# Kernel tuning notes

Hardware: AMD Instinct MI355X
Metric: run time of the kernel (lower is better)

The kernel has to match this reference:

```python
import jax, jax.numpy as jnp
import numpy as np

N, E = 10000, 160000          # nodes, edges
MUL = 128                     # channel multiplicity of 0e and 1o blocks
NSP = 10                      # node_attrs (species one-hot) dim
NRAD = 8                      # edge_feats radial basis dim
SILU_C = 1.6790               # e3nn normalize2mom constant for SiLU
AVG_NEIGH = 16.0
SQ3 = np.sqrt(3.0).astype(np.float32)


def setup_inputs() -> dict:
    key = jax.random.key(0)
    ks = jax.random.split(key, 14)
    d = {}
    d["node_feats"] = jax.random.normal(ks[0], (N, 4 * MUL), jnp.float32)   # [N, 128 + 128*3]
    d["node_attrs"] = jax.random.normal(ks[1], (N, NSP), jnp.float32)
    d["edge_feats"] = jax.random.normal(ks[2], (E, NRAD), jnp.float32)
    d["edge_attrs"] = jax.random.normal(ks[3], (E, 4), jnp.float32)          # [0e | 1o]
    d["edge_index"] = jax.random.randint(ks[4], (2, E), 0, N, jnp.int32)
    # e3nn internal weights are standard normal; normalization applied in forward
    d["lin1_ws"] = jax.random.normal(ks[5], (MUL, MUL), jnp.float32)
    d["lin1_wv"] = jax.random.normal(ks[6], (MUL, MUL), jnp.float32)
    d["fc_w0"] = jax.random.normal(ks[7], (NRAD, 64), jnp.float32)
    d["fc_w1"] = jax.random.normal(ks[8], (64, 64), jnp.float32)
    d["fc_w2"] = jax.random.normal(ks[9], (64, 4 * MUL), jnp.float32)        # tp.weight_numel = 512
    d["lin2_ws"] = jax.random.normal(ks[10], (2 * MUL, MUL), jnp.float32)    # 256x0e -> 128x0e
    d["lin2_wv"] = jax.random.normal(ks[11], (2 * MUL, MUL), jnp.float32)    # 256x1o -> 128x1o
    d["sc_ws"] = jax.random.normal(ks[12], (MUL, NSP, MUL), jnp.float32)
    d["sc_wv"] = jax.random.normal(ks[13], (MUL, NSP, MUL), jnp.float32)
    return d


def _fc(ef, w0, w1, w2):
    # e3nn FullyConnectedNet: x @ W / sqrt(fan_in), normalize2mom-scaled SiLU between layers
    h = SILU_C * jax.nn.silu(ef @ w0 / np.float32(np.sqrt(NRAD)))
    h = SILU_C * jax.nn.silu(h @ w1 / np.float32(8.0))
    return h @ w2 / np.float32(8.0)


def reference(node_feats, node_attrs, edge_feats, edge_attrs, edge_index,
              lin1_ws, lin1_wv, fc_w0, fc_w1, fc_w2,
              lin2_ws, lin2_wv, sc_ws, sc_wv):
    x_s = node_feats[:, :MUL]                       # [N, 128] scalar block
    x_v = node_feats[:, MUL:].reshape(N, MUL, 3)    # [N, 128, 3] vector block

    # self-connection: FullyConnectedTensorProduct with 10x0e attrs; path weight 1/sqrt(mul1*mul2)
    sc_norm = np.float32(1.0 / np.sqrt(MUL * NSP))
    sc_s = jnp.einsum('nu,nv,uvw->nw', x_s, node_attrs, sc_ws) * sc_norm
    sc_v = jnp.einsum('nuc,nv,uvw->nwc', x_v, node_attrs, sc_wv) * sc_norm

    # linear_1 (per-irrep channel mixing, fan_in = 128)
    l1 = np.float32(1.0 / np.sqrt(MUL))
    y_s = (x_s @ lin1_ws) * l1
    y_v = jnp.einsum('nuc,uw->nwc', x_v, lin1_wv) * l1

    src = edge_index[1]
    dst = edge_index[0]
    xs_e = y_s[src]                                 # [E, 128]
    xv_e = y_v[src]                                 # [E, 128, 3]
    a_s = edge_attrs[:, :1]                         # [E, 1]
    a_v = edge_attrs[:, 1:]                         # [E, 3]

    w = _fc(edge_feats, fc_w0, fc_w1, fc_w2)        # [E, 512]
    w_ss, w_sv, w_vs, w_vv = jnp.split(w, 4, axis=1)  # instruction order in source

    # 'uvu' weighted tensor product with e3nn component/element normalization:
    # net coefficient per path works out to 1 except 1o x 1o -> 0e which is 1/sqrt(3)
    mid_s0 = w_ss * xs_e * a_s                                          # 0e*0e->0e
    mid_s1 = w_vv * jnp.einsum('euc,ec->eu', xv_e, a_v) / SQ3           # 1o*1o->0e
    mid_v2 = (w_sv * xs_e)[:, :, None] * a_v[:, None, :]                # 0e*1o->1o
    mid_v3 = w_vs[:, :, None] * xv_e * a_s[:, :, None]                  # 1o*0e->1o

    inv = np.float32(1.0 / np.sqrt(AVG_NEIGH))
    s = jax.ops.segment_sum(jnp.concatenate([mid_s0, mid_s1], axis=1), dst, num_segments=N) * inv  # [N, 256]
    v = jax.ops.segment_sum(jnp.concatenate([mid_v2, mid_v3], axis=1), dst, num_segments=N) * inv  # [N, 256, 3]

    # linear_2 (fan_in = 256)
    l2 = np.float32(1.0 / np.sqrt(2 * MUL))
    out_s = (s @ lin2_ws) * l2 + sc_s
    out_v = jnp.einsum('nuc,uw->nwc', v, lin2_wv) * l2 + sc_v

    return jnp.concatenate([out_s, out_v.reshape(N, 3 * MUL)], axis=1)   # [N, 512]
```

## Files before the change

### kernel.cpp

```cpp
#include <hip/hip_runtime.h>
#include <hip/hip_bf16.h>
#include <math.h>

#define N_NODES 10000
#define N_EDGES 160000
#define SO_BLK 157
#define VO_BLK 469

typedef __attribute__((ext_vector_type(8))) short short8x;
typedef __attribute__((ext_vector_type(4))) float floatx4;
typedef __attribute__((ext_vector_type(4))) unsigned int uint4x;
typedef __attribute__((ext_vector_type(2))) unsigned int uint2x;

union S8 { short8x v; unsigned short u[8]; uint4 q; uint4x qx; };
union U2 { uint2x v; unsigned short us[4]; };

__device__ __forceinline__ unsigned short f2bf(float x) {
    unsigned int u = __float_as_uint(x);
    return (unsigned short)((u + 0x7fffu + ((u >> 16) & 1u)) >> 16);
}
__device__ __forceinline__ float bf2f(unsigned short u) {
    return __uint_as_float(((unsigned)u) << 16);
}
__device__ __forceinline__ float silu_c(float x) {
    return 1.679f * x / (1.0f + __expf(-x));
}

__global__ __launch_bounds__(256) void pack_all_kernel(
    const float* __restrict__ sc_ws, const float* __restrict__ lin2_ws,
    const float* __restrict__ sc_wv, const float* __restrict__ lin2_wv,
    const float* __restrict__ fc_w2, const float* __restrict__ fc_w1,
    const float* __restrict__ lin1_ws, const float* __restrict__ lin1_wv,
    unsigned short* __restrict__ b_pre, unsigned short* __restrict__ w2a,
    unsigned short* __restrict__ w1a, unsigned short* __restrict__ b_lin)
{
    const int bid = blockIdx.x;
    const int t = threadIdx.x;
    if (bid < 192) {
        int id = bid * 256 + t;
        int mat = id / 24576;
        int slot = id - mat * 24576;
        int ks = slot >> 9;
        int rr = slot & 511;
        int lane = rr & 63;
        int quad = lane >> 4;
        int n = ((rr >> 6) << 4) + (lane & 15);
        const float* sc  = mat ? sc_wv  : sc_ws;
        const float* lin = mat ? lin2_wv : lin2_ws;
        S8 pk;
        #pragma unroll
        for (int j = 0; j < 8; j++) {
            int k = ks * 32 + quad * 8 + j;
            float w;
            if (k < 1280) {
                int u = k & 127, v = k >> 7;
                w = sc[(u * 10 + v) * 128 + n];
            } else {
                w = lin[(k - 1280) * 128 + n];
            }
            pk.u[j] = f2bf(w);
        }
        *(uint4*)(b_pre + (size_t)id * 8) = pk.q;
    } else if (bid < 208) {
        int id = (bid - 192) * 256 + t;
        int lane = id & 63;
        int mfg = (id >> 6) & 31;
        int ks = id >> 11;
        int col = mfg * 16 + (lane & 15);
        int k0 = ks * 32 + (lane >> 4) * 8;
        S8 pk;
        #pragma unroll
        for (int j = 0; j < 8; j++)
            pk.u[j] = f2bf(fc_w2[(k0 + j) * 512 + col] * 0.125f);
        *(uint4*)(w2a + (size_t)id * 8) = pk.q;
    } else if (bid < 210) {
        int id = (bid - 208) * 256 + t;
        int lane = id & 63;
        int mf = (id >> 6) & 3;
        int ks = id >> 8;
        int m = mf * 16 + (lane & 15);
        int k0 = ks * 32 + (lane >> 4) * 8;
        S8 pk;
        #pragma unroll
        for (int j = 0; j < 8; j++)
            pk.u[j] = f2bf(fc_w1[(k0 + j) * 64 + m] * 0.125f);
        *(uint4*)(w1a + (size_t)id * 8) = pk.q;
    } else {
        int id = (bid - 210) * 256 + t;
        int mat = id >> 11;
        int slot = id & 2047;
        int ks = slot >> 9;
        int rr = slot & 511;
        int nf = rr >> 6;
        int lane = rr & 63;
        int n = nf * 16 + (lane & 15);
        int k0 = ks * 32 + (lane >> 4) * 8;
        const float* w = mat ? lin1_wv : lin1_ws;
        const float l1 = 0.0883883476483f;
        S8 pk;
        #pragma unroll
        for (int j = 0; j < 8; j++)
            pk.u[j] = f2bf(w[(k0 + j) * 128 + n] * l1);
        *(uint4*)(b_lin + (size_t)id * 8) = pk.q;
    }
}

__global__ __launch_bounds__(256) void node_lin1_mfma(
    const float* __restrict__ node_feats,
    const unsigned short* __restrict__ b_lin,
    unsigned short* __restrict__ y_pk,
    unsigned short* __restrict__ xvP16)
{
    __shared__ __align__(16) unsigned char smem[32768];
    short8x* Al = (short8x*)smem;
    unsigned short* Yt = (unsigned short*)smem;

    const int blk = blockIdx.x;
    const int t = threadIdx.x;
    const int base = blk * 32;
    const int lane = t & 63;
    const int wv = t >> 6;
    const int m15 = lane & 15;
    const int k0q = (lane >> 4) * 8;

    #pragma unroll
    for (int it = 0; it < 8; it++) {
        int g = wv * 8 + it;
        int af = g >> 2;
        int ks = g & 3;
        int m = af * 16 + m15;
        int comp = m >> 5;
        int nloc = m & 31;
        int node = base + nloc;
        int valid = (node < N_NODES);
        if (!valid) node = N_NODES - 1;
        int k0 = ks * 32 + k0q;
        const float* row = node_feats + (size_t)node * 512;
        S8 pk;
        if (comp == 0) {
            float4 a = *(const float4*)&row[k0];
            float4 b = *(const float4*)&row[k0 + 4];
            pk.u[0] = f2bf(a.x); pk.u[1] = f2bf(a.y); pk.u[2] = f2bf(a.z); pk.u[3] = f2bf(a.w);
            pk.u[4] = f2bf(b.x); pk.u[5] = f2bf(b.y); pk.u[6] = f2bf(b.z); pk.u[7] = f2bf(b.w);
        } else {
            int c = comp - 1;
            #pragma unroll
            for (int j = 0; j < 8; j++)
                pk.u[j] = f2bf(row[128 + (k0 + j) * 3 + c]);
            if (valid)
                *(uint4*)&xvP16[((size_t)node * 3 + c) * 128 + k0] = pk.q;
        }
        Al[(ks * 8 + af) * 64 + lane] = pk.v;
    }
    __syncthreads();

    floatx4 c[8][2];
    #pragma unroll
    for (int af = 0; af < 8; af++) {
        c[af][0] = (floatx4){0.f, 0.f, 0.f, 0.f};
        c[af][1] = (floatx4){0.f, 0.f, 0.f, 0.f};
    }

    const uint4* bq = (const uint4*)b_lin;
    #pragma unroll
    for (int ks = 0; ks < 4; ks++) {
        S8 bs0, bs1, bv0, bv1;
        bs0.q = bq[       ks*512 + (wv*2+0)*64 + lane];
        bs1.q = bq[       ks*512 + (wv*2+1)*64 + lane];
        bv0.q = bq[2048 + ks*512 + (wv*2+0)*64 + lane];
        bv1.q = bq[2048 + ks*512 + (wv*2+1)*64 + lane];
        #pragma unroll
        for (int af = 0; af < 8; af++) {
            short8x a = Al[(ks*8 + af)*64 + lane];
            if (af < 2) {
                c[af][0] = __builtin_amdgcn_mfma_f32_16x16x32_bf16(a, bs0.v, c[af][0], 0, 0, 0);
                c[af][1] = __builtin_amdgcn_mfma_f32_16x16x32_bf16(a, bs1.v, c[af][1], 0, 0, 0);
            } else {
                c[af][0] = __builtin_amdgcn_mfma_f32_16x16x32_bf16(a, bv0.v, c[af][0], 0, 0, 0);
                c[af][1] = __builtin_amdgcn_mfma_f32_16x16x32_bf16(a, bv1.v, c[af][1], 0, 0, 0);
            }
        }
    }
    __syncthreads();

    {
        const int rq = (lane >> 4) * 4;
        #pragma unroll
        for (int af = 0; af < 8; af++) {
            #pragma unroll
            for (int nf = 0; nf < 2; nf++) {
                int u = wv * 32 + nf * 16 + m15;
                #pragma unroll
                for (int i = 0; i < 4; i++) {
                    int m = af * 16 + rq + i;
                    int comp = m >> 5, nloc = m & 31;
                    Yt[(nloc * 128 + u) * 4 + comp] = f2bf(c[af][nf][i]);
                }
            }
        }
    }
    __syncthreads();
    {
        unsigned short* dst = y_pk + (size_t)base * 512;
        int nrem = N_NODES - base;
        #pragma unroll
        for (int it = 0; it < 8; it++) {
            int idx = it * 256 + t;
            if ((idx >> 6) < nrem)
                *(uint4*)(dst + (size_t)idx * 8) = *(const uint4*)&Yt[idx * 8];
        }
    }
}

__global__ __launch_bounds__(256) void hist_kernel(const int* __restrict__ edge_index,
                                                   int* __restrict__ deg) {
    int e = blockIdx.x * 256 + threadIdx.x;
    if (e < N_EDGES) atomicAdd(&deg[edge_index[e]], 1);
}

__global__ __launch_bounds__(1024) void scan_kernel(const int* __restrict__ deg,
                                                    int* __restrict__ row_start,
                                                    int* __restrict__ cursor) {
    __shared__ int wsum[16];
    __shared__ int carry_s;
    const int t = threadIdx.x;
    const int lane = t & 63, w = t >> 6;
    if (t == 0) carry_s = 0;
    __syncthreads();
    for (int chunk = 0; chunk < 10; chunk++) {
        int idx = chunk * 1024 + t;
        int v = (idx < N_NODES) ? deg[idx] : 0;
        int x = v;
        #pragma unroll
        for (int off = 1; off < 64; off <<= 1) {
            int yv = __shfl_up(x, off, 64);
            if (lane >= off) x += yv;
        }
        if (lane == 63) wsum[w] = x;
        __syncthreads();
        int wpre = 0;
        for (int i = 0; i < w; i++) wpre += wsum[i];
        int incl = x + wpre + carry_s;
        int excl = incl - v;
        if (idx < N_NODES) { row_start[idx] = excl; cursor[idx] = excl; }
        __syncthreads();
        if (t == 1023) carry_s = incl;
        __syncthreads();
    }
    if (t == 0) row_start[N_NODES] = carry_s;
}

__global__ __launch_bounds__(256) void scatter_kernel(const int* __restrict__ edge_index,
                                                      const float* __restrict__ edge_attrs,
                                                      int* __restrict__ cursor,
                                                      int* __restrict__ edge_list,
                                                      int* __restrict__ srcs,
                                                      float* __restrict__ ea_sorted) {
    int e = blockIdx.x * 256 + threadIdx.x;
    if (e < N_EDGES) {
        int pos = atomicAdd(&cursor[edge_index[e]], 1);
        edge_list[pos] = e;
        srcs[pos] = edge_index[N_EDGES + e];
        float4 ea = *(const float4*)(edge_attrs + (size_t)e * 4);
        *(float4*)(ea_sorted + (size_t)pos * 4) = ea;
    }
}

__global__ __launch_bounds__(256) void edge_w_mfma(
    const float* __restrict__ edge_feats,
    const int* __restrict__ edge_list,
    const float* __restrict__ fc_w0,
    const unsigned short* __restrict__ w1a,
    const unsigned short* __restrict__ w2a,
    unsigned short* __restrict__ w_pk)
{
    __shared__ __align__(16) unsigned char smem[26368];
    float* ef = (float*)smem;
    unsigned short* h0b = (unsigned short*)(smem + 2304);
    unsigned short* T   = (unsigned short*)smem;
    unsigned short* h1b = (unsigned short*)(smem + 16896);
    int* eids = (int*)(smem + 26112);

    const int blk = blockIdx.x;
    const int t = threadIdx.x;
    const int eb0 = blk * 64;
    const int lane = t & 63;
    const int wv = t >> 6;
    const int quad = lane >> 4;
    const int m15 = lane & 15;

    if (t < 64) eids[t] = edge_list[eb0 + t];
    __syncthreads();

    #pragma unroll
    for (int r = 0; r < 2; r++) {
        int idx = r * 256 + t;
        int el = idx >> 3;
        int k = idx & 7;
        ef[el * 9 + k] = edge_feats[(size_t)eids[el] * 8 + k];
    }
    __syncthreads();

    {
        const int e_loc = t >> 2;
        const int c0 = (t & 3) * 16;
        float a0[16];
        #pragma unroll
        for (int i = 0; i < 16; i++) a0[i] = 0.f;
        const float* efr = &ef[e_loc * 9];
        #pragma unroll
        for (int k = 0; k < 8; k++) {
            float ek = efr[k];
            float w[16];
            #pragma unroll
            for (int q4 = 0; q4 < 4; q4++)
                *(float4*)&w[q4*4] = *(const float4*)&fc_w0[k*64 + c0 + q4*4];
            #pragma unroll
            for (int i = 0; i < 16; i++) a0[i] += ek * w[i];
        }
        const float is8 = 0.35355339059f;
        S8 p0, p1;
        #pragma unroll
        for (int i = 0; i < 8; i++) {
            p0.u[i] = f2bf(silu_c(a0[i] * is8));
            p1.u[i] = f2bf(silu_c(a0[8 + i] * is8));
        }
        *(uint4*)&h0b[e_loc * 72 + c0]     = p0.q;
        *(uint4*)&h0b[e_loc * 72 + c0 + 8] = p1.q;
    }
    __syncthreads();

    {
        floatx4 c2[4];
        #pragma unroll
        for (int ee = 0; ee < 4; ee++) c2[ee] = (floatx4){0.f, 0.f, 0.f, 0.f};
        const uint4* w1aq = (const uint4*)w1a;
        #pragma unroll
        for (int ks = 0; ks < 2; ks++) {
            S8 afr;
            afr.q = w1aq[(ks*4 + wv)*64 + lane];
            #pragma unroll
            for (int ee = 0; ee < 4; ee++) {
                S8 bfr;
                bfr.q = *(const uint4*)&h0b[(ee*16 + m15) * 72 + ks*32 + quad*8];
                c2[ee] = __builtin_amdgcn_mfma_f32_16x16x32_bf16(afr.v, bfr.v, c2[ee], 0, 0, 0);
            }
        }
        #pragma unroll
        for (int ee = 0; ee < 4; ee++) {
            ushort4 pk = make_ushort4(f2bf(silu_c(c2[ee][0])), f2bf(silu_c(c2[ee][1])),
                                      f2bf(silu_c(c2[ee][2])), f2bf(silu_c(c2[ee][3])));
            *(ushort4*)&h1b[(ee*16 + m15) * 72 + wv*16 + quad*4] = pk;
        }
    }
    __syncthreads();

    const uint4* w2aq = (const uint4*)w2a;
    #pragma unroll 1
    for (int p = 0; p < 4; p++) {
        floatx4 c3[2][4];
        #pragma unroll
        for (int mf = 0; mf < 2; mf++)
            #pragma unroll
            for (int ee = 0; ee < 4; ee++)
                c3[mf][ee] = (floatx4){0.f, 0.f, 0.f, 0.f};

        #pragma unroll
        for (int ks = 0; ks < 2; ks++) {
            S8 bfr[4];
            #pragma unroll
            for (int ee = 0; ee < 4; ee++)
                bfr[ee].q = *(const uint4*)&h1b[(ee*16 + m15) * 72 + ks*32 + quad*8];
            #pragma unroll
            for (int mf = 0; mf < 2; mf++) {
                S8 afr;
                afr.q = w2aq[(size_t)(ks*32 + wv*8 + p*2 + mf) * 64 + lane];
                #pragma unroll
                for (int ee = 0; ee < 4; ee++)
                    c3[mf][ee] = __builtin_amdgcn_mfma_f32_16x16x32_bf16(afr.v, bfr[ee].v, c3[mf][ee], 0, 0, 0);
            }
        }

        __syncthreads();
        #pragma unroll
        for (int mf = 0; mf < 2; mf++) {
            #pragma unroll
            for (int ee = 0; ee < 4; ee++) {
                int e = ee*16 + m15;
                #pragma unroll
                for (int i = 0; i < 4; i++) {
                    int colp = mf*16 + quad*4 + i;
                    T[e*132 + colp*4 + wv] = f2bf(c3[mf][ee][i]);
                }
            }
        }
        __syncthreads();

        #pragma unroll
        for (int it = 0; it < 8; it++) {
            int idx = it * 256 + t;
            int e  = idx >> 5;
            int cu = idx & 31;
            uint2x v = *(const uint2x*)&T[e*132 + cu*4];
            unsigned short* dstp = w_pk + ((size_t)(eb0 + e) * 128 + p*32 + cu) * 4;
            *(uint2x*)dstp = v;
        }
    }
}

__global__ __launch_bounds__(256) void gather_kernel(
    const int* __restrict__ row_start,
    const int* __restrict__ srcs,
    const float* __restrict__ ea_sorted,
    const unsigned short* __restrict__ w_pk,
    const unsigned short* __restrict__ y_pk,
    float* __restrict__ accS,
    float* __restrict__ accV)
{
    const int t = threadIdx.x;
    const int wv = t >> 6;
    const int n = blockIdx.x * 2 + (wv >> 1);
    const int lane = t & 63;
    const int u = ((wv & 1) << 6) + lane;

    const int eb = row_start[n];
    const int ee = row_start[n + 1];

    float aS0=0.f, aS1=0.f;
    float aV2x=0.f, aV2y=0.f, aV2z=0.f;
    float aV3x=0.f, aV3y=0.f, aV3z=0.f;

    auto consume = [&](const U2& w8, const U2& y8, const float4& ea) {
        float wss = bf2f(w8.us[0]), wsv = bf2f(w8.us[1]);
        float wvs = bf2f(w8.us[2]), wvv = bf2f(w8.us[3]);
        float qs = bf2f(y8.us[0]), q0 = bf2f(y8.us[1]), q1 = bf2f(y8.us[2]), q2 = bf2f(y8.us[3]);
        aS0 += wss * qs * ea.x;
        aS1 += wvv * (q0*ea.y + q1*ea.z + q2*ea.w);
        float tsv = wsv * qs;
        aV2x += tsv * ea.y; aV2y += tsv * ea.z; aV2z += tsv * ea.w;
        float tvs = wvs * ea.x;
        aV3x += tvs * q0; aV3y += tvs * q1; aV3z += tvs * q2;
    };

    if (eb < ee) {
        const int lastE = ee - 1;
        int j1 = (eb+1 < lastE) ? eb+1 : lastE;
        int sA = srcs[eb];
        int sB = srcs[j1];
        int sP0 = srcs[(eb+2 < lastE) ? eb+2 : lastE];
        int sP1 = srcs[(eb+3 < lastE) ? eb+3 : lastE];

        U2 wA, wB, yA, yB; float4 eaA, eaB;
        wA.v = __builtin_nontemporal_load((const uint2x*)(w_pk + ((size_t)eb * 128 + u) * 4));
        eaA  = *(const float4*)(ea_sorted + (size_t)eb * 4);
        yA.v = *(const uint2x*)(y_pk + ((size_t)sA * 128 + u) * 4);
        wB.v = __builtin_nontemporal_load((const uint2x*)(w_pk + ((size_t)j1 * 128 + u) * 4));
        eaB  = *(const float4*)(ea_sorted + (size_t)j1 * 4);
        yB.v = *(const uint2x*)(y_pk + ((size_t)sB * 128 + u) * 4);

        for (int i = eb; i < ee; i += 2) {
            consume(wA, yA, eaA);
            {
                int jn = (i+2 < lastE) ? i+2 : lastE;
                wA.v = __builtin_nontemporal_load((const uint2x*)(w_pk + ((size_t)jn * 128 + u) * 4));
                eaA  = *(const float4*)(ea_sorted + (size_t)jn * 4);
                yA.v = *(const uint2x*)(y_pk + ((size_t)sP0 * 128 + u) * 4);
                sP0 = srcs[(i+4 < lastE) ? i+4 : lastE];
            }
            if (i + 1 < ee) consume(wB, yB, eaB);
            {
                int jn = (i+3 < lastE) ? i+3 : lastE;
                wB.v = __builtin_nontemporal_load((const uint2x*)(w_pk + ((size_t)jn * 128 + u) * 4));
                eaB  = *(const float4*)(ea_sorted + (size_t)jn * 4);
                yB.v = *(const uint2x*)(y_pk + ((size_t)sP1 * 128 + u) * 4);
                sP1 = srcs[(i+5 < lastE) ? i+5 : lastE];
            }
        }
    }

    const float inv = 0.25f;
    const float s1c = 0.57735026919f * 0.25f;
    accS[(size_t)n*256 + u]       = aS0 * inv;
    accS[(size_t)n*256 + 128 + u] = aS1 * s1c;
    accV[((size_t)n*3+0)*256 + u]       = aV2x * inv;
    accV[((size_t)n*3+0)*256 + 128 + u] = aV3x * inv;
    accV[((size_t)n*3+1)*256 + u]       = aV2y * inv;
    accV[((size_t)n*3+1)*256 + 128 + u] = aV3y * inv;
    accV[((size_t)n*3+2)*256 + u]       = aV2z * inv;
    accV[((size_t)n*3+2)*256 + 128 + u] = aV3z * inv;
}

__global__ __launch_bounds__(256) void node_out_mfma(
    const float* __restrict__ node_feats,
    const float* __restrict__ node_attrs,
    const unsigned short* __restrict__ xvP16,
    const float* __restrict__ accS,
    const float* __restrict__ accV,
    const unsigned short* __restrict__ b_pre,
    float* __restrict__ out)
{
    __shared__ __align__(16) short8x Abuf[2][256];
    const int bid = blockIdx.x;
    const int t = threadIdx.x;
    const int lane = t & 63;
    const int wv = t >> 6;
    const bool is_s = (bid < SO_BLK);

    const int r    = ((t >> 6) << 4) + (t & 15);
    const int q8   = ((t >> 4) & 3) * 8;

    const float* px = nullptr;
    const unsigned short* pxv = nullptr;
    const float* pa;
    const float* pat;
    if (is_s) {
        int R = bid * 64 + r;
        int node = (R < N_NODES) ? R : 0;
        px  = node_feats + (size_t)node * 512;
        pa  = accS + (size_t)node * 256;
        pat = node_attrs + node * 10;
    } else {
        int Rg = (bid - SO_BLK) * 64 + r;
        if (Rg >= 3 * N_NODES) Rg = 0;
        int node = Rg / 3;
        pxv = xvP16 + (size_t)Rg * 128;
        pa  = accV + (size_t)Rg * 256;
        pat = node_attrs + node * 10;
    }

    const uint4* bb = (const uint4*)(b_pre) + (is_s ? 0 : 24576);
    const float sc_norm = 0.02795084972f;
    const float l2 = 0.0625f;

    float xf[4][8];
    S8    xh[4];
    if (is_s) {
        #pragma unroll
        for (int c = 0; c < 4; c++) {
            floatx4 lo = *(const floatx4*)&px[c*32 + q8];
            floatx4 hi = *(const floatx4*)&px[c*32 + q8 + 4];
            #pragma unroll
            for (int i = 0; i < 4; i++) { xf[c][i] = lo[i]; xf[c][4+i] = hi[i]; }
        }
    } else {
        #pragma unroll
        for (int c = 0; c < 4; c++)
            xh[c].q = *(const uint4*)&pxv[c*32 + q8];
    }
    float attC = pat[0] * sc_norm;

    floatx4 acc[4][2];
    #pragma unroll
    for (int af = 0; af < 4; af++) {
        acc[af][0] = (floatx4){0.f, 0.f, 0.f, 0.f};
        acc[af][1] = (floatx4){0.f, 0.f, 0.f, 0.f};
    }

    const int cof0 = (wv*2+0)*64 + lane;
    const int cof1 = (wv*2+1)*64 + lane;

    auto packx = [&](int c_, float att_) -> short8x {
        S8 pk;
        if (is_s) {
            #pragma unroll
            for (int i = 0; i < 8; i++) pk.u[i] = f2bf(xf[c_][i] * att_);
        } else {
            #pragma unroll
            for (int i = 0; i < 8; i++) pk.u[i] = f2bf(bf2f(xh[c_].u[i]) * att_);
        }
        return pk.v;
    };
    auto mstep = [&](int kb, const S8& b0, const S8& b1) {
        __builtin_amdgcn_s_setprio(1);
        #pragma unroll
        for (int af = 0; af < 4; af++) {
            short8x a = Abuf[kb][af*64 + lane];
            acc[af][0] = __builtin_amdgcn_mfma_f32_16x16x32_bf16(a, b0.v, acc[af][0], 0, 0, 0);
            acc[af][1] = __builtin_amdgcn_mfma_f32_16x16x32_bf16(a, b1.v, acc[af][1], 0, 0, 0);
        }
        __builtin_amdgcn_s_setprio(0);
    };
    auto bload = [&](int k2, S8& b0, S8& b1) {
        b0.q = bb[(size_t)k2*512 + cof0];
        b1.q = bb[(size_t)k2*512 + cof1];
    };
    auto barrier_ = [&]() {
        asm volatile("s_waitcnt lgkmcnt(0)" ::: "memory");
        __builtin_amdgcn_s_barrier();
    };

    S8 bA0, bA1, bB0, bB1;
    bload(0, bA0, bA1);
    bload(1, bB0, bB1);

    Abuf[0][t] = packx(0, attC);
    barrier_();

    #pragma unroll 1
    for (int vb = 0; vb < 9; vb++) {
        float attN = pat[vb + 1] * sc_norm;
        const int ksb = vb * 4;
        Abuf[1][t] = packx(1, attC); mstep(0, bA0, bA1); bload(ksb+2, bA0, bA1); barrier_();
        Abuf[0][t] = packx(2, attC); mstep(1, bB0, bB1); bload(ksb+3, bB0, bB1); barrier_();
        Abuf[1][t] = packx(3, attC); mstep(0, bA0, bA1); bload(ksb+4, bA0, bA1); barrier_();
        Abuf[0][t] = packx(0, attN); mstep(1, bB0, bB1); bload(ksb+5, bB0, bB1); barrier_();
        attC = attN;
    }

    floatx4 aT0[2], aT1[2];
    auto issue0 = [&](int k_) { int j2 = (k_-40)*32 + q8;
        aT0[0] = *(const floatx4*)&pa[j2]; aT0[1] = *(const floatx4*)&pa[j2+4]; };
    auto issue1 = [&](int k_) { int j2 = (k_-40)*32 + q8;
        aT1[0] = *(const floatx4*)&pa[j2]; aT1[1] = *(const floatx4*)&pa[j2+4]; };
    auto packT = [&](const floatx4* a2) -> short8x {
        S8 pk;
        #pragma unroll
        for (int i = 0; i < 4; i++) { pk.u[i] = f2bf(a2[0][i] * l2); pk.u[4+i] = f2bf(a2[1][i] * l2); }
        return pk.v;
    };

    Abuf[1][t] = packx(1, attC); mstep(0, bA0, bA1); bload(38, bA0, bA1); barrier_();
    Abuf[0][t] = packx(2, attC); mstep(1, bB0, bB1); bload(39, bB0, bB1); barrier_();
    issue0(40);
    Abuf[1][t] = packx(3, attC); mstep(0, bA0, bA1); bload(40, bA0, bA1); barrier_();
    issue1(41);
    Abuf[0][t] = packT(aT0); mstep(1, bB0, bB1); bload(41, bB0, bB1); barrier_();
    issue0(42);
    Abuf[1][t] = packT(aT1); mstep(0, bA0, bA1); bload(42, bA0, bA1); barrier_();
    issue1(43);
    Abuf[0][t] = packT(aT0); mstep(1, bB0, bB1); bload(43, bB0, bB1); barrier_();
    issue0(44);
    Abuf[1][t] = packT(aT1); mstep(0, bA0, bA1); bload(44, bA0, bA1); barrier_();
    issue1(45);
    Abuf[0][t] = packT(aT0); mstep(1, bB0, bB1); bload(45, bB0, bB1); barrier_();
    issue0(46);
    Abuf[1][t] = packT(aT1); mstep(0, bA0, bA1); bload(46, bA0, bA1); barrier_();
    issue1(47);
    Abuf[0][t] = packT(aT0); mstep(1, bB0, bB1); bload(47, bB0, bB1); barrier_();
    Abuf[1][t] = packT(aT1); mstep(0, bA0, bA1); barrier_();
    mstep(1, bB0, bB1);

    const int m = lane & 15;
    const int rq = (lane >> 4) * 4;
    if (is_s) {
        const int n0 = bid * 64;
        #pragma unroll
        for (int af = 0; af < 4; af++) {
            #pragma unroll
            for (int i = 0; i < 4; i++) {
                int n = n0 + af*16 + rq + i;
                if (n < N_NODES) {
                    out[(size_t)n*512 + wv*32 + m]      = acc[af][0][i];
                    out[(size_t)n*512 + wv*32 + 16 + m] = acc[af][1][i];
                }
            }
        }
    } else {
        const int r0 = (bid - SO_BLK) * 64;
        #pragma unroll
        for (int af = 0; af < 4; af++) {
            #pragma unroll
            for (int i = 0; i < 4; i++) {
                int Rg = r0 + af*16 + rq + i;
                if (Rg < 3 * N_NODES) {
                    int nn = Rg / 3;
                    int cc = Rg - nn * 3;
                    float* po = out + (size_t)nn*512 + 128 + cc;
                    po[(wv*32 + m)*3]      = acc[af][0][i];
                    po[(wv*32 + 16 + m)*3] = acc[af][1][i];
                }
            }
        }
    }
}

extern "C" void kernel_launch(void* const* d_in, const int* in_sizes, int n_in,
                              void* d_out, int out_size, void* d_ws, size_t ws_size,
                              hipStream_t stream) {
    const float* node_feats = (const float*)d_in[0];
    const float* node_attrs = (const float*)d_in[1];
    const float* edge_feats = (const float*)d_in[2];
    const float* edge_attrs = (const float*)d_in[3];
    const int*   edge_index = (const int*)  d_in[4];
    const float* lin1_ws    = (const float*)d_in[5];
    const float* lin1_wv    = (const float*)d_in[6];
    const float* fc_w0      = (const float*)d_in[7];
    const float* fc_w1      = (const float*)d_in[8];
    const float* fc_w2      = (const float*)d_in[9];
    const float* lin2_ws    = (const float*)d_in[10];
    const float* lin2_wv    = (const float*)d_in[11];
    const float* sc_ws      = (const float*)d_in[12];
    const float* sc_wv      = (const float*)d_in[13];
    float* out = (float*)d_out;

    unsigned short* y_pk  = (unsigned short*)d_ws;
    float* accS = (float*)(y_pk + (size_t)5120000);
    float* accV = accS + (size_t)2560000;
    unsigned short* xvP16 = (unsigned short*)(accV + (size_t)7680000);
    unsigned short* w_pk  = xvP16 + (size_t)3840000;
    int* deg       = (int*)(w_pk + (size_t)81920000);
    int* row_start = deg + 10016;
    int* cursor    = row_start + 10016;
    int* edge_list = cursor + 10016;
    int* srcs      = edge_list + N_EDGES;
    float* ea_sorted = (float*)(srcs + N_EDGES);
    unsigned short* b_pre = (unsigned short*)(ea_sorted + (size_t)N_EDGES * 4);
    unsigned short* w2a   = b_pre + (size_t)2 * 24576 * 8;
    unsigned short* w1a   = w2a + (size_t)4096 * 8;
    unsigned short* b_lin = w1a + (size_t)512 * 8;
    const size_t need = (size_t)5120000 * 2 + (size_t)(2560000 + 7680000) * 4
                      + (size_t)3840000 * 2 + (size_t)81920000 * 2
                      + (size_t)(10016 * 3 + N_EDGES * 2) * 4
                      + (size_t)N_EDGES * 4 * 4
                      + ((size_t)2 * 24576 * 8 + (size_t)4096 * 8 + (size_t)512 * 8
                         + (size_t)4096 * 8) * 2;
    if (ws_size < need) return;

    hipLaunchKernelGGL(pack_all_kernel, dim3(226), dim3(256), 0, stream,
                       sc_ws, lin2_ws, sc_wv, lin2_wv, fc_w2, fc_w1, lin1_ws, lin1_wv,
                       b_pre, w2a, w1a, b_lin);
    hipLaunchKernelGGL(node_lin1_mfma, dim3(313), dim3(256), 0, stream,
                       node_feats, b_lin, y_pk, xvP16);

    hipMemsetAsync(deg, 0, (size_t)N_NODES * sizeof(int), stream);
    hipLaunchKernelGGL(hist_kernel, dim3(625), dim3(256), 0, stream, edge_index, deg);
    hipLaunchKernelGGL(scan_kernel, dim3(1), dim3(1024), 0, stream, deg, row_start, cursor);
    hipLaunchKernelGGL(scatter_kernel, dim3(625), dim3(256), 0, stream,
                       edge_index, edge_attrs, cursor, edge_list, srcs, ea_sorted);
    hipLaunchKernelGGL(edge_w_mfma, dim3(2500), dim3(256), 0, stream,
                       edge_feats, edge_list, fc_w0, w1a, w2a, w_pk);
    hipLaunchKernelGGL(gather_kernel, dim3(5000), dim3(256), 0, stream,
                       row_start, srcs, ea_sorted, w_pk, y_pk, accS, accV);

    hipLaunchKernelGGL(node_out_mfma, dim3(SO_BLK + VO_BLK), dim3(256), 0, stream,
                       node_feats, node_attrs, xvP16, accS, accV, b_pre, out);
}
```

Baseline: 289.9 us.

## Fuse per-edge weight MLP into node-segment gather, dropping w_pk buffer

The edge radial MLP kernel and the gather kernel become one kernel. Each block owns 8 destination nodes and processes their contiguous CSR edge range in 64-edge tiles. Tensor-product weights are kept in shared memory and consumed immediately instead of being written to and re-read from a 164MB global w_pk buffer. The costs are less parallelism (one 32-lane group per node handling 32 channels per pass), extra barriers per pass, and load imbalance across blocks with uneven degree.

After: 536.2 us. +85.0%, slower.

```diff
diff --git a/kernel.cpp b/kernel.cpp
--- a/kernel.cpp
+++ b/kernel.cpp
@@ -13,7 +13,8 @@
 typedef __attribute__((ext_vector_type(2))) unsigned int uint2x;
 
 union S8 { short8x v; unsigned short u[8]; uint4 q; uint4x qx; };
-union U2 { uint2x v; unsigned short us[4]; };
+
+template<int N> struct ic { static constexpr int value = N; };
 
 __device__ __forceinline__ unsigned short f2bf(float x) {
     unsigned int u = __float_as_uint(x);
@@ -266,228 +267,241 @@
     }
 }
 
-__global__ __launch_bounds__(256) void edge_w_mfma(
+__global__ __launch_bounds__(256) void edge_w_fused(
     const float* __restrict__ edge_feats,
     const int* __restrict__ edge_list,
+    const int* __restrict__ srcs,
+    const float* __restrict__ ea_sorted,
+    const int* __restrict__ row_start,
     const float* __restrict__ fc_w0,
     const unsigned short* __restrict__ w1a,
     const unsigned short* __restrict__ w2a,
-    unsigned short* __restrict__ w_pk)
+    const unsigned short* __restrict__ y_pk,
+    float* __restrict__ accS,
+    float* __restrict__ accV)
 {
-    __shared__ __align__(16) unsigned char smem[26368];
+    __shared__ __align__(16) unsigned char smem[27712];
     float* ef = (float*)smem;
     unsigned short* h0b = (unsigned short*)(smem + 2304);
     unsigned short* T   = (unsigned short*)smem;
     unsigned short* h1b = (unsigned short*)(smem + 16896);
-    int* eids = (int*)(smem + 26112);
-
-    const int blk = blockIdx.x;
+    int* eids   = (int*)(smem + 26112);
+    int* srcs_l = (int*)(smem + 26368);
+    float* ea_l = (float*)(smem + 26624);
+    int* rs_l   = (int*)(smem + 27648);
+
+    const int b = blockIdx.x;
     const int t = threadIdx.x;
-    const int eb0 = blk * 64;
+    const int n0 = b * 8;
     const int lane = t & 63;
     const int wv = t >> 6;
     const int quad = lane >> 4;
     const int m15 = lane & 15;
-
-    if (t < 64) eids[t] = edge_list[eb0 + t];
+    const int u_loc = t & 31;
+    const int nd = t >> 5;
+
+    if (t < 9) rs_l[t] = row_start[n0 + t];
     __syncthreads();
-
+    const int eb = rs_l[0], ee = rs_l[8];
+    const int nlo = rs_l[nd], nhi = rs_l[nd + 1];
+    const int ntiles = (ee > eb) ? ((ee - eb + 63) >> 6) : 0;
+
+    float acc[4][8];
     #pragma unroll
-    for (int r = 0; r < 2; r++) {
-        int idx = r * 256 + t;
-        int el = idx >> 3;
-        int k = idx & 7;
-        ef[el * 9 + k] = edge_feats[(size_t)eids[el] * 8 + k];
-    }
-    __syncthreads();
-
-    {
-        const int e_loc = t >> 2;
-        const int c0 = (t & 3) * 16;
-        float a0[16];
-        #pragma unroll
-        for (int i = 0; i < 16; i++) a0[i] = 0.f;
-        const float* efr = &ef[e_loc * 9];
-        #pragma unroll
-        for (int k = 0; k < 8; k++) {
-            float ek = efr[k];
-            float w[16];
-            #pragma unroll
-            for (int q4 = 0; q4 < 4; q4++)
-                *(float4*)&w[q4*4] = *(const float4*)&fc_w0[k*64 + c0 + q4*4];
-            #pragma unroll
-            for (int i = 0; i < 16; i++) a0[i] += ek * w[i];
-        }
-        const float is8 = 0.35355339059f;
-        S8 p0, p1;
-        #pragma unroll
-        for (int i = 0; i < 8; i++) {
-            p0.u[i] = f2bf(silu_c(a0[i] * is8));
-            p1.u[i] = f2bf(silu_c(a0[8 + i] * is8));
-        }
-        *(uint4*)&h0b[e_loc * 72 + c0]     = p0.q;
-        *(uint4*)&h0b[e_loc * 72 + c0 + 8] = p1.q;
-    }
-    __syncthreads();
-
-    {
-        floatx4 c2[4];
-        #pragma unroll
-        for (int ee = 0; ee < 4; ee++) c2[ee] = (floatx4){0.f, 0.f, 0.f, 0.f};
-        const uint4* w1aq = (const uint4*)w1a;
-        #pragma unroll
-        for (int ks = 0; ks < 2; ks++) {
-            S8 afr;
-            afr.q = w1aq[(ks*4 + wv)*64 + lane];
-            #pragma unroll
-            for (int ee = 0; ee < 4; ee++) {
-                S8 bfr;
-                bfr.q = *(const uint4*)&h0b[(ee*16 + m15) * 72 + ks*32 + quad*8];
-                c2[ee] = __builtin_amdgcn_mfma_f32_16x16x32_bf16(afr.v, bfr.v, c2[ee], 0, 0, 0);
-            }
-        }
-        #pragma unroll
-        for (int ee = 0; ee < 4; ee++) {
-            ushort4 pk = make_ushort4(f2bf(silu_c(c2[ee][0])), f2bf(silu_c(c2[ee][1])),
-                                      f2bf(silu_c(c2[ee][2])), f2bf(silu_c(c2[ee][3])));
-            *(ushort4*)&h1b[(ee*16 + m15) * 72 + wv*16 + quad*4] = pk;
-        }
-    }
-    __syncthreads();
-
+    for (int p = 0; p < 4; p++)
+        #pragma unroll
+        for (int k = 0; k < 8; k++) acc[p][k] = 0.f;
+
+    auto consume1 = [&](float* a8, ushort4 w4, ushort4 y4, const float4& ea) {
+        float wss = bf2f(w4.x), wsv = bf2f(w4.y);
+        float wvs = bf2f(w4.z), wvv = bf2f(w4.w);
+        float qs = bf2f(y4.x), q0 = bf2f(y4.y), q1 = bf2f(y4.z), q2 = bf2f(y4.w);
+        a8[0] += wss * qs * ea.x;
+        a8[1] += wvv * (q0*ea.y + q1*ea.z + q2*ea.w);
+        float tsv = wsv * qs;
+        a8[2] += tsv * ea.y; a8[3] += tsv * ea.z; a8[4] += tsv * ea.w;
+        float tvs = wvs * ea.x;
+        a8[5] += tvs * q0; a8[6] += tvs * q1; a8[7] += tvs * q2;
+    };
+
+    const uint4* w1aq = (const uint4*)w1a;
     const uint4* w2aq = (const uint4*)w2a;
+
     #pragma unroll 1
-    for (int p = 0; p < 4; p++) {
-        floatx4 c3[2][4];
-        #pragma unroll
-        for (int mf = 0; mf < 2; mf++)
-            #pragma unroll
-            for (int ee = 0; ee < 4; ee++)
-                c3[mf][ee] = (floatx4){0.f, 0.f, 0.f, 0.f};
-
-        #pragma unroll
-        for (int ks = 0; ks < 2; ks++) {
-            S8 bfr[4];
-            #pragma unroll
-            for (int ee = 0; ee < 4; ee++)
-                bfr[ee].q = *(const uint4*)&h1b[(ee*16 + m15) * 72 + ks*32 + quad*8];
+    for (int tile = 0; tile < ntiles; tile++) {
+        const int tbeg = eb + (tile << 6);
+        const int tend = (tbeg + 64 < ee) ? tbeg + 64 : ee;
+
+        __syncthreads();
+
+        if (t < 64) {
+            int pos = tbeg + t; if (pos >= ee) pos = ee - 1;
+            eids[t]   = edge_list[pos];
+            srcs_l[t] = srcs[pos];
+        }
+        {
+            int el = t >> 2;
+            int pos = tbeg + el; if (pos >= ee) pos = ee - 1;
+            ea_l[el * 4 + (t & 3)] = ea_sorted[(size_t)pos * 4 + (t & 3)];
+        }
+        __syncthreads();
+
+        #pragma unroll
+        for (int r = 0; r < 2; r++) {
+            int idx = r * 256 + t;
+            int el = idx >> 3;
+            int k = idx & 7;
+            ef[el * 9 + k] = edge_feats[(size_t)eids[el] * 8 + k];
+        }
+        __syncthreads();
+
+        {
+            const int e_loc = t >> 2;
+            const int c0 = (t & 3) * 16;
+            float a0[16];
+            #pragma unroll
+            for (int i = 0; i < 16; i++) a0[i] = 0.f;
+            const float* efr = &ef[e_loc * 9];
+            #pragma unroll
+            for (int k = 0; k < 8; k++) {
+                float ek = efr[k];
+                float w[16];
+                #pragma unroll
+                for (int q4 = 0; q4 < 4; q4++)
+                    *(float4*)&w[q4*4] = *(const float4*)&fc_w0[k*64 + c0 + q4*4];
+                #pragma unroll
+                for (int i = 0; i < 16; i++) a0[i] += ek * w[i];
+            }
+            const float is8 = 0.35355339059f;
+            S8 p0, p1;
+            #pragma unroll
+            for (int i = 0; i < 8; i++) {
+                p0.u[i] = f2bf(silu_c(a0[i] * is8));
+                p1.u[i] = f2bf(silu_c(a0[8 + i] * is8));
+            }
+            *(uint4*)&h0b[e_loc * 72 + c0]     = p0.q;
+            *(uint4*)&h0b[e_loc * 72 + c0 + 8] = p1.q;
+        }
+        __syncthreads();
+
+        {
+            floatx4 c2[4];
+            #pragma unroll
+            for (int ee2 = 0; ee2 < 4; ee2++) c2[ee2] = (floatx4){0.f, 0.f, 0.f, 0.f};
+            #pragma unroll
+            for (int ks = 0; ks < 2; ks++) {
+                S8 afr;
+                afr.q = w1aq[(ks*4 + wv)*64 + lane];
+                #pragma unroll
+                for (int ee2 = 0; ee2 < 4; ee2++) {
+                    S8 bfr;
+                    bfr.q = *(const uint4*)&h0b[(ee2*16 + m15) * 72 + ks*32 + quad*8];
+                    c2[ee2] = __builtin_amdgcn_mfma_f32_16x16x32_bf16(afr.v, bfr.v, c2[ee2], 0, 0, 0);
+                }
+            }
+            #pragma unroll
+            for (int ee2 = 0; ee2 < 4; ee2++) {
+                ushort4 pk = make_ushort4(f2bf(silu_c(c2[ee2][0])), f2bf(silu_c(c2[ee2][1])),
+                                          f2bf(silu_c(c2[ee2][2])), f2bf(silu_c(c2[ee2][3])));
+                *(ushort4*)&h1b[(ee2*16 + m15) * 72 + wv*16 + quad*4] = pk;
+            }
+        }
+        __syncthreads();
+
+        auto do_pass = [&](auto pc) {
+            constexpr int p = decltype(pc)::value;
+            floatx4 c3[2][4];
+            #pragma unroll
+            for (int mf = 0; mf < 2; mf++)
+                #pragma unroll
+                for (int ee2 = 0; ee2 < 4; ee2++)
+                    c3[mf][ee2] = (floatx4){0.f, 0.f, 0.f, 0.f};
+
+            #pragma unroll
+            for (int ks = 0; ks < 2; ks++) {
+                S8 bfr[4];
+                #pragma unroll
+                for (int ee2 = 0; ee2 < 4; ee2++)
+                    bfr[ee2].q = *(const uint4*)&h1b[(ee2*16 + m15) * 72 + ks*32 + quad*8];
+                #pragma unroll
+                for (int mf = 0; mf < 2; mf++) {
+                    S8 afr;
+                    afr.q = w2aq[(size_t)(ks*32 + wv*8 + p*2 + mf) * 64 + lane];
+                    #pragma unroll
+                    for (int ee2 = 0; ee2 < 4; ee2++)
+                        c3[mf][ee2] = __builtin_amdgcn_mfma_f32_16x16x32_bf16(afr.v, bfr[ee2].v, c3[mf][ee2], 0, 0, 0);
+                }
+            }
+
+            __syncthreads();
             #pragma unroll
             for (int mf = 0; mf < 2; mf++) {
-                S8 afr;
-                afr.q = w2aq[(size_t)(ks*32 + wv*8 + p*2 + mf) * 64 + lane];
                 #pragma unroll
-                for (int ee = 0; ee < 4; ee++)
-                    c3[mf][ee] = __builtin_amdgcn_mfma_f32_16x16x32_bf16(afr.v, bfr[ee].v, c3[mf][ee], 0, 0, 0);
-            }
-        }
-
-        __syncthreads();
-        #pragma unroll
-        for (int mf = 0; mf < 2; mf++) {
-            #pragma unroll
-            for (int ee = 0; ee < 4; ee++) {
-                int e = ee*16 + m15;
-                #pragma unroll
-                for (int i = 0; i < 4; i++) {
-                    int colp = mf*16 + quad*4 + i;
-                    T[e*132 + colp*4 + wv] = f2bf(c3[mf][ee][i]);
+                for (int ee2 = 0; ee2 < 4; ee2++) {
+                    int e = ee2*16 + m15;
+                    #pragma unroll
+                    for (int i = 0; i < 4; i++) {
+                        int colp = mf*16 + quad*4 + i;
+                        T[e*132 + colp*4 + wv] = f2bf(c3[mf][ee2][i]);
+                    }
                 }
             }
-        }
-        __syncthreads();
-
-        #pragma unroll
-        for (int it = 0; it < 8; it++) {
-            int idx = it * 256 + t;
-            int e  = idx >> 5;
-            int cu = idx & 31;
-            uint2x v = *(const uint2x*)&T[e*132 + cu*4];
-            unsigned short* dstp = w_pk + ((size_t)(eb0 + e) * 128 + p*32 + cu) * 4;
-            *(uint2x*)dstp = v;
-        }
-    }
-}
-
-__global__ __launch_bounds__(256) void gather_kernel(
-    const int* __restrict__ row_start,
-    const int* __restrict__ srcs,
-    const float* __restrict__ ea_sorted,
-    const unsigned short* __restrict__ w_pk,
-    const unsigned short* __restrict__ y_pk,
-    float* __restrict__ accS,
-    float* __restrict__ accV)
-{
-    const int t = threadIdx.x;
-    const int wv = t >> 6;
-    const int n = blockIdx.x * 2 + (wv >> 1);
-    const int lane = t & 63;
-    const int u = ((wv & 1) << 6) + lane;
-
-    const int eb = row_start[n];
-    const int ee = row_start[n + 1];
-
-    float aS0=0.f, aS1=0.f;
-    float aV2x=0.f, aV2y=0.f, aV2z=0.f;
-    float aV3x=0.f, aV3y=0.f, aV3z=0.f;
-
-    auto consume = [&](const U2& w8, const U2& y8, const float4& ea) {
-        float wss = bf2f(w8.us[0]), wsv = bf2f(w8.us[1]);
-        float wvs = bf2f(w8.us[2]), wvv = bf2f(w8.us[3]);
-        float qs = bf2f(y8.us[0]), q0 = bf2f(y8.us[1]), q1 = bf2f(y8.us[2]), q2 = bf2f(y8.us[3]);
-        aS0 += wss * qs * ea.x;
-        aS1 += wvv * (q0*ea.y + q1*ea.z + q2*ea.w);
-        float tsv = wsv * qs;
-        aV2x += tsv * ea.y; aV2y += tsv * ea.z; aV2z += tsv * ea.w;
-        float tvs = wvs * ea.x;
-        aV3x += tvs * q0; aV3y += tvs * q1; aV3z += tvs * q2;
-    };
-
-    if (eb < ee) {
-        const int lastE = ee - 1;
-        int j1 = (eb+1 < lastE) ? eb+1 : lastE;
-        int sA = srcs[eb];
-        int sB = srcs[j1];
-        int sP0 = srcs[(eb+2 < lastE) ? eb+2 : lastE];
-        int sP1 = srcs[(eb+3 < lastE) ? eb+3 : lastE];
-
-        U2 wA, wB, yA, yB; float4 eaA, eaB;
-        wA.v = __builtin_nontemporal_load((const uint2x*)(w_pk + ((size_t)eb * 128 + u) * 4));
-        eaA  = *(const float4*)(ea_sorted + (size_t)eb * 4);
-        yA.v = *(const uint2x*)(y_pk + ((size_t)sA * 128 + u) * 4);
-        wB.v = __builtin_nontemporal_load((const uint2x*)(w_pk + ((size_t)j1 * 128 + u) * 4));
-        eaB  = *(const float4*)(ea_sorted + (size_t)j1 * 4);
-        yB.v = *(const uint2x*)(y_pk + ((size_t)sB * 128 + u) * 4);
-
-        for (int i = eb; i < ee; i += 2) {
-            consume(wA, yA, eaA);
+            __syncthreads();
+
             {
-                int jn = (i+2 < lastE) ? i+2 : lastE;
-                wA.v = __builtin_nontemporal_load((const uint2x*)(w_pk + ((size_t)jn * 128 + u) * 4));
-                eaA  = *(const float4*)(ea_sorted + (size_t)jn * 4);
-                yA.v = *(const uint2x*)(y_pk + ((size_t)sP0 * 128 + u) * 4);
-                sP0 = srcs[(i+4 < lastE) ? i+4 : lastE];
-            }
-            if (i + 1 < ee) consume(wB, yB, eaB);
-            {
-                int jn = (i+3 < lastE) ? i+3 : lastE;
-                wB.v = __builtin_nontemporal_load((const uint2x*)(w_pk + ((size_t)jn * 128 + u) * 4));
-                eaB  = *(const float4*)(ea_sorted + (size_t)jn * 4);
-                yB.v = *(const uint2x*)(y_pk + ((size_t)sP1 * 128 + u) * 4);
-                sP1 = srcs[(i+5 < lastE) ? i+5 : lastE];
-            }
-        }
+                int lo = (nlo > tbeg) ? nlo : tbeg;
+                int hi = (nhi < tend) ? nhi : tend;
+                int j  = lo - tbeg;
+                int je = hi - tbeg;
+                if (j < je) {
+                    const int u = p * 32 + u_loc;
+                    int j1 = (j + 1 < je) ? j + 1 : j;
+                    ushort4 wA = *(const ushort4*)&T[j*132 + u_loc*4];
+                    ushort4 yA = *(const ushort4*)(y_pk + ((size_t)srcs_l[j]*128 + u)*4);
+                    float4  eA = *(const float4*)&ea_l[j*4];
+                    ushort4 wB = *(const ushort4*)&T[j1*132 + u_loc*4];
+                    ushort4 yB = *(const ushort4*)(y_pk + ((size_t)srcs_l[j1]*128 + u)*4);
+                    float4  eB = *(const float4*)&ea_l[j1*4];
+                    for (; j < je; j += 2) {
+                        consume1(acc[p], wA, yA, eA);
+                        {
+                            int jn = (j + 2 < je) ? j + 2 : j;
+                            wA = *(const ushort4*)&T[jn*132 + u_loc*4];
+                            yA = *(const ushort4*)(y_pk + ((size_t)srcs_l[jn]*128 + u)*4);
+                            eA = *(const float4*)&ea_l[jn*4];
+                        }
+                        if (j + 1 < je) consume1(acc[p], wB, yB, eB);
+                        {
+                            int jm = (j + 3 < je) ? j + 3 : j;
+                            wB = *(const ushort4*)&T[jm*132 + u_loc*4];
+                            yB = *(const ushort4*)(y_pk + ((size_t)srcs_l[jm]*128 + u)*4);
+                            eB = *(const float4*)&ea_l[jm*4];
+                        }
+                    }
+                }
+            }
+        };
+        do_pass(ic<0>{});
+        do_pass(ic<1>{});
+        do_pass(ic<2>{});
+        do_pass(ic<3>{});
     }
 
     const float inv = 0.25f;
     const float s1c = 0.57735026919f * 0.25f;
-    accS[(size_t)n*256 + u]       = aS0 * inv;
-    accS[(size_t)n*256 + 128 + u] = aS1 * s1c;
-    accV[((size_t)n*3+0)*256 + u]       = aV2x * inv;
-    accV[((size_t)n*3+0)*256 + 128 + u] = aV3x * inv;
-    accV[((size_t)n*3+1)*256 + u]       = aV2y * inv;
-    accV[((size_t)n*3+1)*256 + 128 + u] = aV3y * inv;
-    accV[((size_t)n*3+2)*256 + u]       = aV2z * inv;
-    accV[((size_t)n*3+2)*256 + 128 + u] = aV3z * inv;
+    const int n = n0 + nd;
+    #pragma unroll
+    for (int p = 0; p < 4; p++) {
+        int u = p * 32 + u_loc;
+        accS[(size_t)n*256 + u]        = acc[p][0] * inv;
+        accS[(size_t)n*256 + 128 + u]  = acc[p][1] * s1c;
+        accV[((size_t)n*3+0)*256 + u]        = acc[p][2] * inv;
+        accV[((size_t)n*3+1)*256 + u]        = acc[p][3] * inv;
+        accV[((size_t)n*3+2)*256 + u]        = acc[p][4] * inv;
+        accV[((size_t)n*3+0)*256 + 128 + u]  = acc[p][5] * inv;
+        accV[((size_t)n*3+1)*256 + 128 + u]  = acc[p][6] * inv;
+        accV[((size_t)n*3+2)*256 + 128 + u]  = acc[p][7] * inv;
+    }
 }
 
 __global__ __launch_bounds__(256) void node_out_mfma(
@@ -697,8 +711,7 @@
     float* accS = (float*)(y_pk + (size_t)5120000);
     float* accV = accS + (size_t)2560000;
     unsigned short* xvP16 = (unsigned short*)(accV + (size_t)7680000);
-    unsigned short* w_pk  = xvP16 + (size_t)3840000;
-    int* deg       = (int*)(w_pk + (size_t)81920000);
+    int* deg       = (int*)(xvP16 + (size_t)3840000);
     int* row_start = deg + 10016;
     int* cursor    = row_start + 10016;
     int* edge_list = cursor + 10016;
@@ -709,7 +722,7 @@
     unsigned short* w1a   = w2a + (size_t)4096 * 8;
     unsigned short* b_lin = w1a + (size_t)512 * 8;
     const size_t need = (size_t)5120000 * 2 + (size_t)(2560000 + 7680000) * 4
-                      + (size_t)3840000 * 2 + (size_t)81920000 * 2
+                      + (size_t)3840000 * 2
                       + (size_t)(10016 * 3 + N_EDGES * 2) * 4
                       + (size_t)N_EDGES * 4 * 4
                       + ((size_t)2 * 24576 * 8 + (size_t)4096 * 8 + (size_t)512 * 8
@@ -727,10 +740,9 @@
     hipLaunchKernelGGL(scan_kernel, dim3(1), dim3(1024), 0, stream, deg, row_start, cursor);
     hipLaunchKernelGGL(scatter_kernel, dim3(625), dim3(256), 0, stream,
                        edge_index, edge_attrs, cursor, edge_list, srcs, ea_sorted);
-    hipLaunchKernelGGL(edge_w_mfma, dim3(2500), dim3(256), 0, stream,
-                       edge_feats, edge_list, fc_w0, w1a, w2a, w_pk);
-    hipLaunchKernelGGL(gather_kernel, dim3(5000), dim3(256), 0, stream,
-                       row_start, srcs, ea_sorted, w_pk, y_pk, accS, accV);
+    hipLaunchKernelGGL(edge_w_fused, dim3(1250), dim3(256), 0, stream,
+                       edge_feats, edge_list, srcs, ea_sorted, row_start,
+                       fc_w0, w1a, w2a, y_pk, accS, accV);
 
     hipLaunchKernelGGL(node_out_mfma, dim3(SO_BLK + VO_BLK), dim3(256), 0, stream,
                        node_feats, node_attrs, xvP16, accS, accV, b_pre, out);
```
